# Kernel tuning notes

Hardware: AMD Instinct MI355X
Metric: run time of the kernel (lower is better)

The kernel has to match this reference:

```python
import math
import jax, jax.numpy as jnp
import numpy as np

B, T, C = 2, 2048, 1024
H, D = 16, 64
QC, KC = 128, 256
SCALE = 1.0 / math.sqrt(D)


def _int4_linear(x, w_int8, scale, bias):
    # W = dequant(int8) * per-output-channel scale; y = x @ W.T + bias
    w = w_int8.astype(jnp.float32) * scale[:, None]
    return x @ w.T + bias


def _attention_recompute(q, k, v):
    # q,k,v: (B,H,T,D). Williams-style 2D tiling with streaming (online) softmax, causal.
    nq, nk = T // QC, T // KC
    qt = q.reshape(B, H, nq, QC, D).transpose(2, 0, 1, 3, 4)  # (nq,B,H,QC,D)
    kt = k.reshape(B, H, nk, KC, D).transpose(2, 0, 1, 3, 4)  # (nk,B,H,KC,D)
    vt = v.reshape(B, H, nk, KC, D).transpose(2, 0, 1, 3, 4)
    q_idx = jnp.arange(T).reshape(nq, QC)
    k_idx = jnp.arange(T).reshape(nk, KC)

    def per_qchunk(q_tile, q_pos):
        def step(carry, inp):
            m, l, o = carry
            k_c, v_c, k_pos = inp
            s = jnp.einsum('bhqd,bhkd->bhqk', q_tile, k_c) * SCALE
            mask = k_pos[None, None, None, :] <= q_pos[None, None, :, None]
            s = jnp.where(mask, s, -jnp.inf)
            s_max = jnp.max(s, axis=-1, keepdims=True)
            m_new = jnp.maximum(m, s_max)
            alpha = jnp.exp(m - m_new)
            p = jnp.exp(s - m_new)
            o = o * alpha + jnp.einsum('bhqk,bhkd->bhqd', p, v_c)
            l = l * alpha + jnp.sum(p, axis=-1, keepdims=True)
            return (m_new, l, o), None

        m0 = jnp.full((B, H, QC, 1), -jnp.inf, dtype=q_tile.dtype)
        l0 = jnp.zeros((B, H, QC, 1), dtype=q_tile.dtype)
        o0 = jnp.zeros_like(q_tile)
        (m, l, o), _ = jax.lax.scan(step, (m0, l0, o0), (kt, vt, k_idx))
        return o / (l + 1e-8)

    out = jax.vmap(per_qchunk)(qt, q_idx)  # (nq,B,H,QC,D)
    return out.transpose(1, 2, 0, 3, 4).reshape(B, H, T, D)


def _forward(x, wq, sq, bq, wk, sk, bk, wv, sv, bv, wo, so, bo):
    q = _int4_linear(x, wq, sq, bq).reshape(B, T, H, D).transpose(0, 2, 1, 3)
    k = _int4_linear(x, wk, sk, bk).reshape(B, T, H, D).transpose(0, 2, 1, 3)
    v = _int4_linear(x, wv, sv, bv).reshape(B, T, H, D).transpose(0, 2, 1, 3)
    attn = _attention_recompute(q, k, v)
    y = attn.transpose(0, 2, 1, 3).reshape(B, T, C)
    return _int4_linear(y, wo, so, bo)


def setup_inputs() -> dict:
    key = jax.random.key(0)
    ks = jax.random.split(key, 5)
    x = jax.random.normal(ks[0], (B, T, C), dtype=jnp.float32)

    def w(k):
        return jax.random.randint(k, (C, C), -8, 8, dtype=jnp.int8)

    s = 0.005 * jnp.ones((C,), jnp.float32)  # trainable per-channel scale (init shrunk for sane activations)
    b = jnp.zeros((C,), jnp.float32)
    return {
        'x': x,
        'wq': w(ks[1]), 'sq': s, 'bq': b,
        'wk': w(ks[2]), 'sk': s, 'bk': b,
        'wv': w(ks[3]), 'sv': s, 'bv': b,
        'wo': w(ks[4]), 'so': s, 'bo': b,
    }


def reference(x, wq, sq, bq, wk, sk, bk, wv, sv, bv, wo, so, bo):
    return _forward(x, wq, sq, bq, wk, sk, bk, wv, sv, bv, wo, so, bo)
```

## Files before the change

### kernel.cpp

```cpp
#include <hip/hip_runtime.h>
#include <hip/hip_bf16.h>
#include <stdint.h>

#define BB 2
#define TT 2048
#define CC 1024
#define HH 16
#define DD 64
#define MM (BB*TT)

typedef __bf16 bf16x8 __attribute__((ext_vector_type(8)));
typedef float  f32x4  __attribute__((ext_vector_type(4)));
typedef float  f32x16 __attribute__((ext_vector_type(16)));
typedef unsigned short u16;
typedef unsigned int   u32;

__device__ __forceinline__ u16 f2bf(float f) {
  u32 u = __float_as_uint(f);
  return (u16)((u + 0x7fffu + ((u >> 16) & 1u)) >> 16);
}

__device__ __forceinline__ u32 cvt_pk_bf16(float a, float b) {
  u32 r;
  asm("v_cvt_pk_bf16_f32 %0, %1, %2" : "=v"(r) : "v"(a), "v"(b));
  return r;
}

__device__ __forceinline__ void gload_lds16(const u16* g, u16* l) {
  auto gp = (const u32 __attribute__((address_space(1)))*)(uintptr_t)g;
  auto lp = (u32 __attribute__((address_space(3)))*)(u32)(uintptr_t)l;
  __builtin_amdgcn_global_load_lds(gp, lp, 16, 0, 0);
}

__global__ __launch_bounds__(256)
void k_sentinel(float* __restrict__ out, int n) {
  int i = blockIdx.x * 256 + threadIdx.x;
  if (i < n) out[i] = 9999.0f;
}

__global__ __launch_bounds__(256)
void k_convert(const float* __restrict__ x,
               const int* __restrict__ w0, const int* __restrict__ w1,
               const int* __restrict__ w2, const int* __restrict__ w3,
               u16* __restrict__ xb, u16* __restrict__ wb) {
  const int idx = blockIdx.x * 256 + threadIdx.x;
  const int NX = MM * CC / 4;
  if (idx < NX) {
    float4 v = ((const float4*)x)[idx];
    u32 lo = (u32)f2bf(v.x) | ((u32)f2bf(v.y) << 16);
    u32 hi = (u32)f2bf(v.z) | ((u32)f2bf(v.w) << 16);
    ((uint2*)xb)[idx] = make_uint2(lo, hi);
  } else {
    int u = idx - NX;
    int mat = u >> 18;
    int j = u & 262143;
    const int* ws = (mat == 0) ? w0 : (mat == 1) ? w1 : (mat == 2) ? w2 : w3;
    int4 v = ((const int4*)ws)[j];
    u32 lo = (u32)f2bf((float)v.x) | ((u32)f2bf((float)v.y) << 16);
    u32 hi = (u32)f2bf((float)v.z) | ((u32)f2bf((float)v.w) << 16);
    ((uint2*)wb)[(mat << 18) + j] = make_uint2(lo, hi);
  }
}

__device__ __forceinline__ void gemm_core(const u16* __restrict__ Ag,
                                          const u16* __restrict__ Wg,
                                          int brow, int bcol,
                                          u16* As, u16* Bs, f32x4 acc[4][4]) {
  const int tid  = threadIdx.x;
  const int w    = tid >> 6;
  const int lane = tid & 63;
  const int q = lane & 15, g = lane >> 4;
  const int wm = w >> 1, wn = w & 1;

  for (int kt = 0; kt < CC / 32; ++kt) {
    #pragma unroll
    for (int i = 0; i < 2; ++i) {
      int Lg  = i * 256 + tid;
      int row = Lg >> 2, gc = Lg & 3;
      gload_lds16(Ag + (brow + row) * CC + kt * 32 + gc * 8, As + (i * 256 + w * 64) * 8);
      gload_lds16(Wg + (bcol + row) * CC + kt * 32 + gc * 8, Bs + (i * 256 + w * 64) * 8);
    }
    __syncthreads();
    bf16x8 af[4], bff[4];
    #pragma unroll
    for (int a = 0; a < 4; ++a) af[a]  = *(const bf16x8*)&As[(wm * 64 + a * 16 + q) * 32 + g * 8];
    #pragma unroll
    for (int b = 0; b < 4; ++b) bff[b] = *(const bf16x8*)&Bs[(wn * 64 + b * 16 + q) * 32 + g * 8];
    #pragma unroll
    for (int a = 0; a < 4; ++a) {
      #pragma unroll
      for (int b = 0; b < 4; ++b) {
        acc[a][b] = __builtin_amdgcn_mfma_f32_16x16x32_bf16(af[a], bff[b], acc[a][b], 0, 0, 0);
      }
    }
    __syncthreads();
  }
}

__global__ __launch_bounds__(256)
void k_gemm_qkv(const u16* __restrict__ xb, const u16* __restrict__ wb,
                const float* __restrict__ sq, const float* __restrict__ bq,
                const float* __restrict__ sk, const float* __restrict__ bk,
                const float* __restrict__ sv, const float* __restrict__ bv,
                u16* __restrict__ Qo, u16* __restrict__ Ko, u16* __restrict__ Vt) {
  __shared__ u16 As[128 * 32];
  __shared__ u16 Bs[128 * 32];
  const int bid  = blockIdx.x;
  const int brow = (bid & 31) * 128;
  const int ncol = (bid >> 5) * 128;
  const int mat  = ncol >> 10;
  const int bcol = ncol & 1023;
  const u16* W = wb + (mat << 20);

  f32x4 acc[4][4];
  #pragma unroll
  for (int a = 0; a < 4; ++a)
    #pragma unroll
    for (int b = 0; b < 4; ++b) { f32x4 z = {0.f, 0.f, 0.f, 0.f}; acc[a][b] = z; }

  gemm_core(xb, W, brow, bcol, As, Bs, acc);

  const int tid = threadIdx.x;
  const int w = tid >> 6, lane = tid & 63;
  const int q = lane & 15, g = lane >> 4;
  const int wm = w >> 1, wn = w & 1;
  const float* sarr = (mat == 0) ? sq : (mat == 1) ? sk : sv;
  const float* barr = (mat == 0) ? bq : (mat == 1) ? bk : bv;

  #pragma unroll
  for (int bt = 0; bt < 4; ++bt) {
    const int c = bcol + wn * 64 + bt * 16 + q;
    const float sc = sarr[c];
    const float bi = barr[c];
    const int h = c >> 6, d = c & 63;
    #pragma unroll
    for (int a = 0; a < 4; ++a) {
      #pragma unroll
      for (int r = 0; r < 4; ++r) {
        const int m = brow + wm * 64 + a * 16 + 4 * g + r;
        const int b_ = m >> 11, t = m & 2047;
        const u16 val = f2bf(acc[a][bt][r] * sc + bi);
        if (mat == 0)      Qo[(((size_t)(b_ * HH + h) * TT) + t) * DD + d] = val;
        else if (mat == 1) Ko[(((size_t)(b_ * HH + h) * TT) + t) * DD + d] = val;
        else               Vt[((size_t)(b_ * HH + h) * DD + d) * TT + t] = val;
      }
    }
  }
}

__global__ __launch_bounds__(256, 2)
void k_attn(const u16* __restrict__ Q, const u16* __restrict__ K,
            const u16* __restrict__ Vt, u16* __restrict__ Y) {
  __shared__ u16 kbuf[2][64 * 64];
  __shared__ u16 vbuf[2][64 * 64];
  const int tid = threadIdx.x;
  const int w = tid >> 6, lane = tid & 63;
  const int q = lane & 31, hi = lane >> 5;
  const int bid = blockIdx.x;
  const int idx = bid & 255, halfg = bid >> 8;
  const int bh = idx & 31;
  const int t8 = idx >> 5;
  const int tile = halfg ? (15 - t8) : t8;
  const int qbase = tile * 128;
  const int qw = qbase + 32 * w;
  const int qg = qw + q;
  const u16* Qh = Q  + (size_t)bh * TT * DD;
  const u16* Kh = K  + (size_t)bh * TT * DD;
  const u16* Vh = Vt + (size_t)bh * DD * TT;
  const int b_ = bh >> 4, h = bh & 15;
  constexpr float SE = 0.125f * 1.44269504088896340736f;

  bf16x8 qf[4];
  #pragma unroll
  for (int c = 0; c < 4; ++c)
    qf[c] = *(const bf16x8*)&Qh[(qw + q) * DD + 16 * c + 8 * hi];

  f32x16 oacc[2];
  oacc[0] = f32x16{}; oacc[1] = f32x16{};
  float m_run = -1.0e30f;
  float l_vec[8];
  #pragma unroll
  for (int u2 = 0; u2 < 8; ++u2) l_vec[u2] = 0.f;

  const int nkb = 2 * tile + 2;
  const int kb_last_w = (qw + 31) >> 6;

  #define STAGE(BUFI, KBASE)                                                        \
    {                                                                               \
      _Pragma("unroll")                                                             \
      for (int r = 0; r < 2; ++r) {                                                 \
        int g = r * 256 + tid;                                                      \
        int row = g >> 3, cB = (g & 7) << 4;                                        \
        int scB = cB ^ ((row & 7) << 4);                                            \
        gload_lds16(Kh + (size_t)((KBASE) + row) * DD + (scB >> 1),                 \
                    &kbuf[BUFI][(r * 256 + w * 64) * 8]);                           \
      }                                                                             \
      _Pragma("unroll")                                                             \
      for (int r = 0; r < 2; ++r) {                                                 \
        int g = r * 256 + tid;                                                      \
        int row = g >> 3, cB = (g & 7) << 4;                                        \
        int scB = cB ^ ((row & 7) << 4);                                            \
        gload_lds16(Vh + (size_t)row * TT + (KBASE) + (scB >> 1),                   \
                    &vbuf[BUFI][(r * 256 + w * 64) * 8]);                           \
      }                                                                             \
    }

  STAGE(0, 0);
  for (int kb = 0; kb < nkb; ++kb) {
    const int kbase = kb * 64;
    if (kb + 1 < nkb) {
      STAGE((kb + 1) & 1, kbase + 64);
      asm volatile("s_waitcnt vmcnt(4)" ::: "memory");
    } else {
      asm volatile("s_waitcnt vmcnt(0)" ::: "memory");
    }
    __builtin_amdgcn_s_barrier();
    __builtin_amdgcn_sched_barrier(0);

    if (kb <= kb_last_w) {
      const u16* kl = kbuf[kb & 1];
      const u16* vl = vbuf[kb & 1];

      bf16x8 kf[2][4];
      #pragma unroll
      for (int s = 0; s < 2; ++s)
        #pragma unroll
        for (int c = 0; c < 4; ++c) {
          const int row = 32 * s + q, cB = 32 * c + 16 * hi;
          kf[s][c] = *(const bf16x8*)&kl[(row * 128 + (cB ^ ((row & 7) << 4))) >> 1];
        }
      f32x16 sacc[2];
      sacc[0] = f32x16{}; sacc[1] = f32x16{};
      __builtin_amdgcn_s_setprio(1);
      #pragma unroll
      for (int c = 0; c < 4; ++c) {
        sacc[0] = __builtin_amdgcn_mfma_f32_32x32x16_bf16(kf[0][c], qf[c], sacc[0], 0, 0, 0);
        sacc[1] = __builtin_amdgcn_mfma_f32_32x32x16_bf16(kf[1][c], qf[c], sacc[1], 0, 0, 0);
      }
      __builtin_amdgcn_s_setprio(0);

      bf16x8 vf[2][2][2];
      #pragma unroll
      for (int dt = 0; dt < 2; ++dt)
        #pragma unroll
        for (int s = 0; s < 2; ++s)
          #pragma unroll
          for (int c2 = 0; c2 < 2; ++c2) {
            const int row = dt * 32 + q, cB = 64 * s + 32 * c2 + 16 * hi;
            vf[dt][s][c2] = *(const bf16x8*)&vl[(row * 128 + (cB ^ ((row & 7) << 4))) >> 1];
          }

      float sr[32];
      #pragma unroll
      for (int s = 0; s < 2; ++s)
        #pragma unroll
        for (int r = 0; r < 16; ++r) sr[s * 16 + r] = sacc[s][r];
      if (kbase + 63 > qw) {
        #pragma unroll
        for (int s = 0; s < 2; ++s)
          #pragma unroll
          for (int r = 0; r < 16; ++r)
            if (kbase + 32 * s + (r & 3) + 8 * (r >> 2) + 4 * hi > qg)
              sr[s * 16 + r] = -__builtin_inff();
      }
      float mx[16];
      #pragma unroll
      for (int u2 = 0; u2 < 16; ++u2) mx[u2] = fmaxf(sr[u2], sr[u2 + 16]);
      #pragma unroll
      for (int st = 8; st > 0; st >>= 1)
        #pragma unroll
        for (int u2 = 0; u2 < st; ++u2) mx[u2] = fmaxf(mx[u2], mx[u2 + st]);
      const float pmax = fmaxf(mx[0], __shfl_xor(mx[0], 32)) * SE;
      const bool keep = __all(pmax <= m_run + 8.0f);
      const float m_new = keep ? m_run : fmaxf(m_run, pmax);
      const float nm = -m_new;
      float p[32];
      #pragma unroll
      for (int u2 = 0; u2 < 32; ++u2)
        p[u2] = __builtin_amdgcn_exp2f(fmaf(sr[u2], SE, nm));
      if (!keep) {
        const float alpha = __builtin_amdgcn_exp2f(m_run - m_new);
        m_run = m_new;
        oacc[0] *= alpha;
        oacc[1] *= alpha;
        #pragma unroll
        for (int u2 = 0; u2 < 8; ++u2) l_vec[u2] *= alpha;
      }
      float t16[16];
      #pragma unroll
      for (int u2 = 0; u2 < 16; ++u2) t16[u2] = p[u2] + p[u2 + 16];
      #pragma unroll
      for (int u2 = 0; u2 < 8; ++u2) l_vec[u2] += t16[u2] + t16[u2 + 8];

      u32 Aw[8], Bw[8];
      #pragma unroll
      for (int n = 0; n < 8; ++n) {
        const int base = ((n >> 2) * 16) + ((n & 3) << 2);
        Aw[n] = cvt_pk_bf16(p[base + 0], p[base + 1]);
        Bw[n] = cvt_pk_bf16(p[base + 2], p[base + 3]);
      }
      bf16x8 pf[2][2];
      #pragma unroll
      for (int s = 0; s < 2; ++s)
        #pragma unroll
        for (int c2 = 0; c2 < 2; ++c2) {
          const int n0 = 4 * s + 2 * c2;
          u32 x0 = Aw[n0], x2 = Aw[n0 + 1];
          asm volatile("v_permlane32_swap_b32 %0, %1" : "+v"(x0), "+v"(x2));
          u32 x1 = Bw[n0], x3 = Bw[n0 + 1];
          asm volatile("v_permlane32_swap_b32 %0, %1" : "+v"(x1), "+v"(x3));
          union { u32 uw[4]; bf16x8 v; } U;
          U.uw[0] = x0; U.uw[1] = x1; U.uw[2] = x2; U.uw[3] = x3;
          pf[s][c2] = U.v;
        }

      __builtin_amdgcn_s_setprio(1);
      #pragma unroll
      for (int s = 0; s < 2; ++s)
        #pragma unroll
        for (int c2 = 0; c2 < 2; ++c2) {
          oacc[0] = __builtin_amdgcn_mfma_f32_32x32x16_bf16(vf[0][s][c2], pf[s][c2], oacc[0], 0, 0, 0);
          oacc[1] = __builtin_amdgcn_mfma_f32_32x32x16_bf16(vf[1][s][c2], pf[s][c2], oacc[1], 0, 0, 0);
        }
      __builtin_amdgcn_s_setprio(0);
    }

    __builtin_amdgcn_s_barrier();
  }

  float l_run = ((l_vec[0] + l_vec[1]) + (l_vec[2] + l_vec[3]))
              + ((l_vec[4] + l_vec[5]) + (l_vec[6] + l_vec[7]));
  float lt = l_run + __shfl_xor(l_run, 32);
  const float inv = 1.f / (lt + 1e-8f);
  #pragma unroll
  for (int dt = 0; dt < 2; ++dt)
    #pragma unroll
    for (int n = 0; n < 4; ++n) {
      u32 lo  = cvt_pk_bf16(oacc[dt][4 * n + 0] * inv, oacc[dt][4 * n + 1] * inv);
      u32 hi2 = cvt_pk_bf16(oacc[dt][4 * n + 2] * inv, oacc[dt][4 * n + 3] * inv);
      *(uint2*)&Y[(size_t)(b_ * TT + qg) * CC + h * 64 + 32 * dt + 8 * n + 4 * hi]
        = make_uint2(lo, hi2);
    }
  #undef STAGE
}

__global__ __launch_bounds__(256)
void k_gemm_o(const u16* __restrict__ Yb, const u16* __restrict__ Wo,
              const float* __restrict__ so, const float* __restrict__ bo,
              float* __restrict__ out) {
  __shared__ u16 As[128 * 32];
  __shared__ u16 Bs[128 * 32];
  const int bid = blockIdx.x;
  const int brow = (bid & 31) * 128;
  const int bcol = (bid >> 5) * 128;
  f32x4 acc[4][4];
  #pragma unroll
  for (int a = 0; a < 4; ++a)
    #pragma unroll
    for (int b = 0; b < 4; ++b) { f32x4 z = {0.f, 0.f, 0.f, 0.f}; acc[a][b] = z; }

  gemm_core(Yb, Wo, brow, bcol, As, Bs, acc);

  const int tid = threadIdx.x;
  const int w = tid >> 6, lane = tid & 63;
  const int q = lane & 15, g = lane >> 4;
  const int wm = w >> 1, wn = w & 1;
  #pragma unroll
  for (int bt = 0; bt < 4; ++bt) {
    const int c = bcol + wn * 64 + bt * 16 + q;
    const float sc = so[c], bi = bo[c];
    #pragma unroll
    for (int a = 0; a < 4; ++a) {
      const int mbase = brow + wm * 64 + a * 16 + 4 * g;
      #pragma unroll
      for (int r = 0; r < 4; ++r) {
        out[(size_t)(mbase + r) * CC + c] = acc[a][bt][r] * sc + bi;
      }
    }
  }
}

extern "C" void kernel_launch(void* const* d_in, const int* in_sizes, int n_in,
                              void* d_out, int out_size, void* d_ws, size_t ws_size,
                              hipStream_t stream) {
  const float* x  = (const float*)d_in[0];
  const int*   wq = (const int*)d_in[1];
  const float* sq = (const float*)d_in[2];
  const float* bq = (const float*)d_in[3];
  const int*   wk = (const int*)d_in[4];
  const float* sk = (const float*)d_in[5];
  const float* bk = (const float*)d_in[6];
  const int*   wv = (const int*)d_in[7];
  const float* sv = (const float*)d_in[8];
  const float* bv = (const float*)d_in[9];
  const int*   wo = (const int*)d_in[10];
  const float* so = (const float*)d_in[11];
  const float* bo = (const float*)d_in[12];

  const size_t NEED = (40u << 20);
  if (ws_size < NEED) {
    k_sentinel<<<dim3((out_size + 255) / 256), dim3(256), 0, stream>>>((float*)d_out, out_size);
    return;
  }

  char* ws = (char*)d_ws;
  u16* xb = (u16*)(ws);
  u16* wb = (u16*)(ws + (8u  << 20));
  u16* Qb = (u16*)(ws + (16u << 20));
  u16* Kb = (u16*)(ws + (24u << 20));
  u16* Vt = (u16*)(ws + (32u << 20));
  u16* Yb = xb;

  k_convert <<<dim3(8192), dim3(256), 0, stream>>>(x, wq, wk, wv, wo, xb, wb);
  k_gemm_qkv<<<dim3(768),  dim3(256), 0, stream>>>(xb, wb, sq, bq, sk, bk, sv, bv, Qb, Kb, Vt);
  k_attn    <<<dim3(512),  dim3(256), 0, stream>>>(Qb, Kb, Vt, Yb);
  k_gemm_o  <<<dim3(256),  dim3(256), 0, stream>>>(Yb, wb + (3u << 20), so, bo, (float*)d_out);
}
```

Baseline: 115.8 us.

## Split attention into 64-row query tiles with two-wave blocks, longest first

The attention kernel now runs 1024 blocks of 128 threads, each owning a 64-query tile, instead of 512 blocks of 256 threads covering 128 queries. Tiles go in descending query position so the longest causal rows are scheduled first. Wave-level skipping of fully masked key blocks is dropped, because both waves in a block now need the same key range. The aim is less wasted work per block and better load balance, at the cost of each K/V tile staged to LDS being shared by fewer waves, which doubles staging traffic per query.

```diff
diff --git a/kernel.cpp b/kernel.cpp
--- a/kernel.cpp
+++ b/kernel.cpp
@@ -148,7 +148,7 @@
   }
 }
 
-__global__ __launch_bounds__(256, 2)
+__global__ __launch_bounds__(128, 2)
 void k_attn(const u16* __restrict__ Q, const u16* __restrict__ K,
             const u16* __restrict__ Vt, u16* __restrict__ Y) {
   __shared__ u16 kbuf[2][64 * 64];
@@ -157,12 +157,9 @@
   const int w = tid >> 6, lane = tid & 63;
   const int q = lane & 31, hi = lane >> 5;
   const int bid = blockIdx.x;
-  const int idx = bid & 255, halfg = bid >> 8;
-  const int bh = idx & 31;
-  const int t8 = idx >> 5;
-  const int tile = halfg ? (15 - t8) : t8;
-  const int qbase = tile * 128;
-  const int qw = qbase + 32 * w;
+  const int bh = bid & 31;
+  const int v = 31 - (bid >> 5);
+  const int qw = v * 64 + 32 * w;
   const int qg = qw + q;
   const u16* Qh = Q  + (size_t)bh * TT * DD;
   const u16* Kh = K  + (size_t)bh * TT * DD;
@@ -182,26 +179,25 @@
   #pragma unroll
   for (int u2 = 0; u2 < 8; ++u2) l_vec[u2] = 0.f;
 
-  const int nkb = 2 * tile + 2;
-  const int kb_last_w = (qw + 31) >> 6;
+  const int nkb = v + 1;
 
   #define STAGE(BUFI, KBASE)                                                        \
     {                                                                               \
       _Pragma("unroll")                                                             \
-      for (int r = 0; r < 2; ++r) {                                                 \
-        int g = r * 256 + tid;                                                      \
+      for (int r2 = 0; r2 < 4; ++r2) {                                              \
+        int g = r2 * 128 + tid;                                                     \
         int row = g >> 3, cB = (g & 7) << 4;                                        \
         int scB = cB ^ ((row & 7) << 4);                                            \
         gload_lds16(Kh + (size_t)((KBASE) + row) * DD + (scB >> 1),                 \
-                    &kbuf[BUFI][(r * 256 + w * 64) * 8]);                           \
+                    &kbuf[BUFI][(r2 * 128 + w * 64) * 8]);                          \
       }                                                                             \
       _Pragma("unroll")                                                             \
-      for (int r = 0; r < 2; ++r) {                                                 \
-        int g = r * 256 + tid;                                                      \
+      for (int r2 = 0; r2 < 4; ++r2) {                                              \
+        int g = r2 * 128 + tid;                                                     \
         int row = g >> 3, cB = (g & 7) << 4;                                        \
         int scB = cB ^ ((row & 7) << 4);                                            \
         gload_lds16(Vh + (size_t)row * TT + (KBASE) + (scB >> 1),                   \
-                    &vbuf[BUFI][(r * 256 + w * 64) * 8]);                           \
+                    &vbuf[BUFI][(r2 * 128 + w * 64) * 8]);                          \
       }                                                                             \
     }
 
@@ -210,123 +206,122 @@
     const int kbase = kb * 64;
     if (kb + 1 < nkb) {
       STAGE((kb + 1) & 1, kbase + 64);
-      asm volatile("s_waitcnt vmcnt(4)" ::: "memory");
+      asm volatile("s_waitcnt vmcnt(8)" ::: "memory");
     } else {
       asm volatile("s_waitcnt vmcnt(0)" ::: "memory");
     }
     __builtin_amdgcn_s_barrier();
     __builtin_amdgcn_sched_barrier(0);
 
-    if (kb <= kb_last_w) {
-      const u16* kl = kbuf[kb & 1];
-      const u16* vl = vbuf[kb & 1];
-
-      bf16x8 kf[2][4];
-      #pragma unroll
-      for (int s = 0; s < 2; ++s)
-        #pragma unroll
-        for (int c = 0; c < 4; ++c) {
-          const int row = 32 * s + q, cB = 32 * c + 16 * hi;
-          kf[s][c] = *(const bf16x8*)&kl[(row * 128 + (cB ^ ((row & 7) << 4))) >> 1];
-        }
-      f32x16 sacc[2];
-      sacc[0] = f32x16{}; sacc[1] = f32x16{};
-      __builtin_amdgcn_s_setprio(1);
+    const u16* kl = kbuf[kb & 1];
+    const u16* vl = vbuf[kb & 1];
+
+    bf16x8 kf[2][4];
+    #pragma unroll
+    for (int s = 0; s < 2; ++s)
       #pragma unroll
       for (int c = 0; c < 4; ++c) {
-        sacc[0] = __builtin_amdgcn_mfma_f32_32x32x16_bf16(kf[0][c], qf[c], sacc[0], 0, 0, 0);
-        sacc[1] = __builtin_amdgcn_mfma_f32_32x32x16_bf16(kf[1][c], qf[c], sacc[1], 0, 0, 0);
-      }
-      __builtin_amdgcn_s_setprio(0);
-
-      bf16x8 vf[2][2][2];
-      #pragma unroll
-      for (int dt = 0; dt < 2; ++dt)
-        #pragma unroll
-        for (int s = 0; s < 2; ++s)
-          #pragma unroll
-          for (int c2 = 0; c2 < 2; ++c2) {
-            const int row = dt * 32 + q, cB = 64 * s + 32 * c2 + 16 * hi;
-            vf[dt][s][c2] = *(const bf16x8*)&vl[(row * 128 + (cB ^ ((row & 7) << 4))) >> 1];
-          }
-
-      float sr[32];
-      #pragma unroll
-      for (int s = 0; s < 2; ++s)
-        #pragma unroll
-        for (int r = 0; r < 16; ++r) sr[s * 16 + r] = sacc[s][r];
-      if (kbase + 63 > qw) {
-        #pragma unroll
-        for (int s = 0; s < 2; ++s)
-          #pragma unroll
-          for (int r = 0; r < 16; ++r)
-            if (kbase + 32 * s + (r & 3) + 8 * (r >> 2) + 4 * hi > qg)
-              sr[s * 16 + r] = -__builtin_inff();
-      }
-      float mx[16];
-      #pragma unroll
-      for (int u2 = 0; u2 < 16; ++u2) mx[u2] = fmaxf(sr[u2], sr[u2 + 16]);
-      #pragma unroll
-      for (int st = 8; st > 0; st >>= 1)
-        #pragma unroll
-        for (int u2 = 0; u2 < st; ++u2) mx[u2] = fmaxf(mx[u2], mx[u2 + st]);
-      const float pmax = fmaxf(mx[0], __shfl_xor(mx[0], 32)) * SE;
-      const bool keep = __all(pmax <= m_run + 8.0f);
-      const float m_new = keep ? m_run : fmaxf(m_run, pmax);
-      const float nm = -m_new;
-      float p[32];
-      #pragma unroll
-      for (int u2 = 0; u2 < 32; ++u2)
-        p[u2] = __builtin_amdgcn_exp2f(fmaf(sr[u2], SE, nm));
-      if (!keep) {
-        const float alpha = __builtin_amdgcn_exp2f(m_run - m_new);
-        m_run = m_new;
-        oacc[0] *= alpha;
-        oacc[1] *= alpha;
-        #pragma unroll
-        for (int u2 = 0; u2 < 8; ++u2) l_vec[u2] *= alpha;
-      }
-      float t16[16];
-      #pragma unroll
-      for (int u2 = 0; u2 < 16; ++u2) t16[u2] = p[u2] + p[u2 + 16];
-      #pragma unroll
-      for (int u2 = 0; u2 < 8; ++u2) l_vec[u2] += t16[u2] + t16[u2 + 8];
-
-      u32 Aw[8], Bw[8];
-      #pragma unroll
-      for (int n = 0; n < 8; ++n) {
-        const int base = ((n >> 2) * 16) + ((n & 3) << 2);
-        Aw[n] = cvt_pk_bf16(p[base + 0], p[base + 1]);
-        Bw[n] = cvt_pk_bf16(p[base + 2], p[base + 3]);
-      }
-      bf16x8 pf[2][2];
+        const int row = 32 * s + q, cB = 32 * c + 16 * hi;
+        kf[s][c] = *(const bf16x8*)&kl[(row * 128 + (cB ^ ((row & 7) << 4))) >> 1];
+      }
+    f32x16 sacc[2];
+    sacc[0] = f32x16{}; sacc[1] = f32x16{};
+    __builtin_amdgcn_s_setprio(1);
+    #pragma unroll
+    for (int c = 0; c < 4; ++c) {
+      sacc[0] = __builtin_amdgcn_mfma_f32_32x32x16_bf16(kf[0][c], qf[c], sacc[0], 0, 0, 0);
+      sacc[1] = __builtin_amdgcn_mfma_f32_32x32x16_bf16(kf[1][c], qf[c], sacc[1], 0, 0, 0);
+    }
+    __builtin_amdgcn_s_setprio(0);
+
+    bf16x8 vf[2][2][2];
+    #pragma unroll
+    for (int dt = 0; dt < 2; ++dt)
       #pragma unroll
       for (int s = 0; s < 2; ++s)
         #pragma unroll
         for (int c2 = 0; c2 < 2; ++c2) {
-          const int n0 = 4 * s + 2 * c2;
-          u32 x0 = Aw[n0], x2 = Aw[n0 + 1];
-          asm volatile("v_permlane32_swap_b32 %0, %1" : "+v"(x0), "+v"(x2));
-          u32 x1 = Bw[n0], x3 = Bw[n0 + 1];
-          asm volatile("v_permlane32_swap_b32 %0, %1" : "+v"(x1), "+v"(x3));
-          union { u32 uw[4]; bf16x8 v; } U;
-          U.uw[0] = x0; U.uw[1] = x1; U.uw[2] = x2; U.uw[3] = x3;
-          pf[s][c2] = U.v;
+          const int row = dt * 32 + q, cB = 64 * s + 32 * c2 + 16 * hi;
+          vf[dt][s][c2] = *(const bf16x8*)&vl[(row * 128 + (cB ^ ((row & 7) << 4))) >> 1];
         }
 
-      __builtin_amdgcn_s_setprio(1);
+    float sr[32];
+    #pragma unroll
+    for (int s = 0; s < 2; ++s)
+      #pragma unroll
+      for (int rr = 0; rr < 16; ++rr) sr[s * 16 + rr] = sacc[s][rr];
+    if (kbase + 63 > qw) {
       #pragma unroll
       for (int s = 0; s < 2; ++s)
         #pragma unroll
-        for (int c2 = 0; c2 < 2; ++c2) {
-          oacc[0] = __builtin_amdgcn_mfma_f32_32x32x16_bf16(vf[0][s][c2], pf[s][c2], oacc[0], 0, 0, 0);
-          oacc[1] = __builtin_amdgcn_mfma_f32_32x32x16_bf16(vf[1][s][c2], pf[s][c2], oacc[1], 0, 0, 0);
-        }
-      __builtin_amdgcn_s_setprio(0);
-    }
+        for (int rr = 0; rr < 16; ++rr)
+          if (kbase + 32 * s + (rr & 3) + 8 * (rr >> 2) + 4 * hi > qg)
+            sr[s * 16 + rr] = -__builtin_inff();
+    }
+    float mx[16];
+    #pragma unroll
+    for (int u2 = 0; u2 < 16; ++u2) mx[u2] = fmaxf(sr[u2], sr[u2 + 16]);
+    #pragma unroll
+    for (int st = 8; st > 0; st >>= 1)
+      #pragma unroll
+      for (int u2 = 0; u2 < st; ++u2) mx[u2] = fmaxf(mx[u2], mx[u2 + st]);
+    const float pmax = fmaxf(mx[0], __shfl_xor(mx[0], 32)) * SE;
+    const bool keep = __all(pmax <= m_run + 8.0f);
+    const float m_new = keep ? m_run : fmaxf(m_run, pmax);
+    const float nm = -m_new;
+    float p[32];
+    #pragma unroll
+    for (int u2 = 0; u2 < 32; ++u2)
+      p[u2] = __builtin_amdgcn_exp2f(fmaf(sr[u2], SE, nm));
+    if (!keep) {
+      const float alpha = __builtin_amdgcn_exp2f(m_run - m_new);
+      m_run = m_new;
+      oacc[0] *= alpha;
+      oacc[1] *= alpha;
+      #pragma unroll
+      for (int u2 = 0; u2 < 8; ++u2) l_vec[u2] *= alpha;
+    }
+    float t16[16];
+    #pragma unroll
+    for (int u2 = 0; u2 < 16; ++u2) t16[u2] = p[u2] + p[u2 + 16];
+    #pragma unroll
+    for (int u2 = 0; u2 < 8; ++u2) l_vec[u2] += t16[u2] + t16[u2 + 8];
+
+    u32 Aw[8], Bw[8];
+    #pragma unroll
+    for (int n = 0; n < 8; ++n) {
+      const int base = ((n >> 2) * 16) + ((n & 3) << 2);
+      Aw[n] = cvt_pk_bf16(p[base + 0], p[base + 1]);
+      Bw[n] = cvt_pk_bf16(p[base + 2], p[base + 3]);
+    }
+    bf16x8 pf[2][2];
+    #pragma unroll
+    for (int s = 0; s < 2; ++s)
+      #pragma unroll
+      for (int c2 = 0; c2 < 2; ++c2) {
+        const int n0 = 4 * s + 2 * c2;
+        u32 x0 = Aw[n0], x2 = Aw[n0 + 1];
+        asm volatile("v_permlane32_swap_b32 %0, %1" : "+v"(x0), "+v"(x2));
+        u32 x1 = Bw[n0], x3 = Bw[n0 + 1];
+        asm volatile("v_permlane32_swap_b32 %0, %1" : "+v"(x1), "+v"(x3));
+        union { u32 uw[4]; bf16x8 vv; } U;
+        U.uw[0] = x0; U.uw[1] = x1; U.uw[2] = x2; U.uw[3] = x3;
+        pf[s][c2] = U.vv;
+      }
+
+    __builtin_amdgcn_s_setprio(1);
+    #pragma unroll
+    for (int s = 0; s < 2; ++s)
+      #pragma unroll
+      for (int c2 = 0; c2 < 2; ++c2) {
+        oacc[0] = __builtin_amdgcn_mfma_f32_32x32x16_bf16(vf[0][s][c2], pf[s][c2], oacc[0], 0, 0, 0);
+        oacc[1] = __builtin_amdgcn_mfma_f32_32x32x16_bf16(vf[1][s][c2], pf[s][c2], oacc[1], 0, 0, 0);
+      }
+    __builtin_amdgcn_s_setprio(0);
 
     __builtin_amdgcn_s_barrier();
   }
+  #undef STAGE
 
   float l_run = ((l_vec[0] + l_vec[1]) + (l_vec[2] + l_vec[3]))
               + ((l_vec[4] + l_vec[5]) + (l_vec[6] + l_vec[7]));
@@ -341,7 +336,6 @@
       *(uint2*)&Y[(size_t)(b_ * TT + qg) * CC + h * 64 + 32 * dt + 8 * n + 4 * hi]
         = make_uint2(lo, hi2);
     }
-  #undef STAGE
 }
 
 __global__ __launch_bounds__(256)
@@ -413,6 +407,6 @@
 
   k_convert <<<dim3(8192), dim3(256), 0, stream>>>(x, wq, wk, wv, wo, xb, wb);
   k_gemm_qkv<<<dim3(768),  dim3(256), 0, stream>>>(xb, wb, sq, bq, sk, bk, sv, bv, Qb, Kb, Vt);
-  k_attn    <<<dim3(512),  dim3(256), 0, stream>>>(Qb, Kb, Vt, Yb);
+  k_attn    <<<dim3(1024), dim3(128), 0, stream>>>(Qb, Kb, Vt, Yb);
   k_gemm_o  <<<dim3(256),  dim3(256), 0, stream>>>(Yb, wb + (3u << 20), so, bo, (float*)d_out);
 }
```

After: 117.4 us. Within noise of the previous version (+1.4%).
